# Kernel optimization log

Hardware: AMD Instinct MI355X
Metric: run time of the kernel (lower is better)

## Reference

```python
import jax, jax.numpy as jnp
import numpy as np

VOCAB, H, L, B, T = 32000, 256, 10, 256, 512


def setup_inputs() -> dict:
    key = jax.random.key(0)
    ks = jax.random.split(key, 6)
    s = 1.0 / np.sqrt(H)
    return {
        "tokens": jax.random.randint(ks[0], (B, T), 0, VOCAB),
        "hidden0": jnp.zeros((L, B, H), jnp.float32),
        "emb": jax.random.normal(ks[1], (VOCAB, H), jnp.float32),
        "Wx_w": jax.random.normal(ks[2], (L, H, H), jnp.float32) * s,
        "Wx_b": jax.random.normal(ks[3], (L, H), jnp.float32) * s,
        "Wh_w": jax.random.normal(ks[4], (L, H, H), jnp.float32) * s,
        "Wh_b": jax.random.normal(ks[5], (L, H), jnp.float32) * s,
    }


def reference(tokens, hidden0, emb, Wx_w, Wx_b, Wh_w, Wh_b):
    # tokens: [B,T] int; hidden0: [L,B,H]; weights stacked over layers.
    embedded = emb[tokens]                    # [B,T,H]
    xs = jnp.swapaxes(embedded, 0, 1)         # [T,B,H]

    def time_step(h, x_t):                    # h: [L,B,H], x_t: [B,H]
        def layer_step(x, layer):
            wx, bx, wh, bh, hl = layer
            # torch Linear: y = x @ W.T + b
            new_h = jnp.tanh(x @ wx.T + bx + hl @ wh.T + bh)
            return new_h, new_h
        x_out, new_h = jax.lax.scan(layer_step, x_t, (Wx_w, Wx_b, Wh_w, Wh_b, h))
        return new_h, x_out                   # carry new hidden stack, emit top-layer output

    h_final, outs = jax.lax.scan(time_step, hidden0, xs)  # outs: [T,B,H]
    return jnp.swapaxes(outs, 0, 1), h_final  # ([B,T,H], [L,B,H])
```

## Files before the change

### kernel.cpp

```cpp
#include <hip/hip_runtime.h>

#define HDIM   256
#define NLAYER 10
#define BATCH  256
#define TSTEPS 512
#define NTHR   512
#define DEPTH  8
#define NCH    160
#define NWG    160

typedef __attribute__((ext_vector_type(8))) short short8;
typedef __attribute__((ext_vector_type(4))) float f32x4;

__device__ __forceinline__ unsigned short bf16_rne(float f) {
    unsigned v = __float_as_uint(f);
    unsigned r = v + 0x7FFFu + ((v >> 16) & 1u);
    return (unsigned short)(r >> 16);
}
__device__ __forceinline__ float bf16_f(unsigned short b) {
    return __uint_as_float(((unsigned)b) << 16);
}
__device__ __forceinline__ float fast_tanh(float v) {
    float a = fabsf(v);
    float e = __expf(-2.0f * a);
    float r = (1.0f - e) / (1.0f + e);
    return __builtin_copysignf(r, v);
}
__device__ __forceinline__ void cvt8(const float* __restrict__ p, short8& hi, short8& lo) {
#pragma unroll
    for (int e = 0; e < 8; ++e) {
        float f = p[e];
        unsigned short h = bf16_rne(f);
        hi[e] = (short)h;
        lo[e] = (short)bf16_rne(f - bf16_f(h));
    }
}
__device__ __forceinline__ void cvtq(unsigned long long q0, unsigned long long q1,
                                     unsigned long long q2, unsigned long long q3,
                                     short8& hi, short8& lo) {
    unsigned long long q[4] = { q0, q1, q2, q3 };
#pragma unroll
    for (int i = 0; i < 4; ++i) {
#pragma unroll
        for (int j = 0; j < 2; ++j) {
            const float f = __uint_as_float((unsigned)(q[i] >> (32 * j)));
            const unsigned short h = bf16_rne(f);
            hi[2 * i + j] = (short)h;
            lo[2 * i + j] = (short)bf16_rne(f - bf16_f(h));
        }
    }
}
__device__ __forceinline__ void unpack8(unsigned long long q0, unsigned long long q1,
                                        unsigned long long q2, unsigned long long q3,
                                        short8& hi, short8& lo) {
    unsigned long long q[4] = { q0, q1, q2, q3 };
#pragma unroll
    for (int i = 0; i < 4; ++i) {
        unsigned u0 = (unsigned)q[i], u1 = (unsigned)(q[i] >> 32);
        hi[2 * i]     = (short)(u0 & 0xffffu); lo[2 * i]     = (short)(u0 >> 16);
        hi[2 * i + 1] = (short)(u1 & 0xffffu); lo[2 * i + 1] = (short)(u1 >> 16);
    }
}

#define MFMA16(a, b, c) __builtin_amdgcn_mfma_f32_16x16x32_bf16((a), (b), (c), 0, 0, 0)

__device__ __forceinline__ void wait_ge(int* f, int need) {
    while (__hip_atomic_load(f, __ATOMIC_RELAXED, __HIP_MEMORY_SCOPE_AGENT) < need)
        __builtin_amdgcn_s_sleep(1);
}
#define AT_LD(p)    __hip_atomic_load((p), __ATOMIC_RELAXED, __HIP_MEMORY_SCOPE_AGENT)
#define AT_ST(p, v) __hip_atomic_store((p), (v), __ATOMIC_RELAXED, __HIP_MEMORY_SCOPE_AGENT)
#define VMDRAIN()   asm volatile("s_waitcnt vmcnt(0)" ::: "memory")

#define WXH 0
#define HHI 131072
#define HLO 139264
#define XHI 147456
#define XLO 155648

__global__ void __launch_bounds__(NTHR, 1) rnn_fused(
    const int* __restrict__ tokens, const float* __restrict__ hidden0,
    const float* __restrict__ emb,
    const float* __restrict__ Wx_w, const float* __restrict__ Wx_b,
    const float* __restrict__ Wh_w, const float* __restrict__ Wh_b,
    unsigned* __restrict__ hg,
    int* __restrict__ fh,
    float* __restrict__ out) {
    const int bid = blockIdx.x;
    const int l = bid >> 4;
    const int s16 = bid & 15;
    const int c = bid;
    const int tid = threadIdx.x;
    const int wv = tid >> 6;
    const int lane = tid & 63;
    const int ln15 = lane & 15;
    const int kq = (lane >> 4) << 3;
    const int hi16 = (lane >> 4) << 4;
    const int swz = (ln15 & 7) << 4;
    const int srow = tid >> 5;
    const int scb = tid & 31;

    __shared__ char smem[163840];
    float* hfinal = out + (size_t)BATCH * TSTEPS * HDIM;

    {
        const float* wxsrcA = Wx_w + (size_t)l * 65536;
        for (int i = 0; i < 16; ++i) {
            const int ch = tid + i * NTHR;
            const int r = ch >> 5, kb = ch & 31;
            short8 hi, lo;
            cvt8(wxsrcA + (size_t)r * HDIM + kb * 8, hi, lo);
            *(short8*)(smem + WXH + r * 512 + ((kb * 16) ^ ((r & 7) << 4))) = hi;
        }
    }
    short8 whh[2][8], whl[2][8], wxl[2][8];
    {
        const float* whsrc = Wh_w + (size_t)l * 65536;
        const float* wxsrc = Wx_w + (size_t)l * 65536;
#define WINIT(ni, kc) do { \
        short8 _d; \
        cvt8(whsrc + (size_t)(wv * 32 + ni * 16 + ln15) * HDIM + kc * 32 + kq, whh[ni][kc], whl[ni][kc]); \
        cvt8(wxsrc + (size_t)(wv * 32 + ni * 16 + ln15) * HDIM + kc * 32 + kq, _d, wxl[ni][kc]); \
        asm volatile("" : "+v"(whh[ni][kc]), "+v"(whl[ni][kc]), "+v"(wxl[ni][kc])); \
    } while (0)
        WINIT(0,0); WINIT(0,1); WINIT(0,2); WINIT(0,3);
        WINIT(0,4); WINIT(0,5); WINIT(0,6); WINIT(0,7);
        WINIT(1,0); WINIT(1,1); WINIT(1,2); WINIT(1,3);
        WINIT(1,4); WINIT(1,5); WINIT(1,6); WINIT(1,7);
#undef WINIT
    }
    {
        short8 hi, lo;
        cvt8(hidden0 + ((size_t)(l * BATCH + s16 * 16 + srow)) * HDIM + scb * 8, hi, lo);
        const int so = srow * 512 + ((scb * 16) ^ ((srow & 7) << 4));
        *(short8*)(smem + HHI + so) = hi;
        *(short8*)(smem + HLO + so) = lo;
    }
    float bv[2];
#pragma unroll
    for (int ni = 0; ni < 2; ++ni) {
        const int col = wv * 32 + ni * 16 + ln15;
        bv[ni] = Wx_b[l * HDIM + col] + Wh_b[l * HDIM + col];
    }

    int* fhme = fh + (size_t)c * TSTEPS;
    int* fhp = (l > 0) ? fh + (size_t)(c - 16) * TSTEPS : nullptr;
    int* fhn = (l < NLAYER - 1) ? fh + (size_t)(c + 16) * TSTEPS : nullptr;

    if (l > 0) {
        if (tid == 0) wait_ge(fhp + 0, 1);
        __syncthreads();
        unsigned long long* xp = (unsigned long long*)
            (hg + ((size_t)0 * NCH + (c - 16)) * 4096) + (size_t)tid * 4;
        unsigned long long q0 = AT_LD(xp), q1 = AT_LD(xp + 1),
                           q2 = AT_LD(xp + 2), q3 = AT_LD(xp + 3);
        short8 sxh, sxl;
        unpack8(q0, q1, q2, q3, sxh, sxl);
        const int so = srow * 512 + ((scb * 16) ^ ((srow & 7) << 4));
        *(short8*)(smem + XHI + so) = sxh;
        *(short8*)(smem + XLO + so) = sxl;
    } else {
        const int tok = tokens[(s16 * 16 + srow) * TSTEPS + 0];
        const float* ep = emb + (size_t)tok * HDIM + scb * 8;
        short8 sxh, sxl;
        cvt8(ep, sxh, sxl);
        const int so = srow * 512 + ((scb * 16) ^ ((srow & 7) << 4));
        *(short8*)(smem + XHI + so) = sxh;
        *(short8*)(smem + XLO + so) = sxl;
    }
    __syncthreads();

    for (int t = 0; t < TSTEPS; ++t) {
        if (tid == 0 && l > 0 && t + 1 < TSTEPS) wait_ge(fhp + (t + 1), 1);
        if (tid == 64 && fhn && t >= 9) wait_ge(fhn + (t - 9), 1);
        __syncthreads();

        unsigned long long q0 = 0, q1 = 0, q2 = 0, q3 = 0;
        if (t + 1 < TSTEPS) {
            if (l > 0) {
                unsigned long long* xp = (unsigned long long*)
                    (hg + ((size_t)((t + 1) % DEPTH) * NCH + (c - 16)) * 4096) + (size_t)tid * 4;
                q0 = AT_LD(xp); q1 = AT_LD(xp + 1); q2 = AT_LD(xp + 2); q3 = AT_LD(xp + 3);
            } else {
                const int tok = tokens[(s16 * 16 + srow) * TSTEPS + (t + 1)];
                const unsigned long long* ep =
                    (const unsigned long long*)(emb + (size_t)tok * HDIM + scb * 8);
                q0 = ep[0]; q1 = ep[1]; q2 = ep[2]; q3 = ep[3];
            }
        }

        f32x4 acc0 = {}, acc1 = {};
#define HX_KC(kc) do { \
        const int _off = ((kc) * 64 + hi16) ^ swz; \
        const short8 hh  = *(const short8*)(smem + HHI + ln15 * 512 + _off); \
        const short8 hl  = *(const short8*)(smem + HLO + ln15 * 512 + _off); \
        const short8 xh  = *(const short8*)(smem + XHI + ln15 * 512 + _off); \
        const short8 xl  = *(const short8*)(smem + XLO + ln15 * 512 + _off); \
        const short8 bh0 = *(const short8*)(smem + WXH + (wv * 32 + ln15) * 512 + _off); \
        const short8 bh1 = *(const short8*)(smem + WXH + (wv * 32 + 16 + ln15) * 512 + _off); \
        acc0 = MFMA16(hh, whh[0][kc], acc0);  acc1 = MFMA16(hh, whh[1][kc], acc1); \
        acc0 = MFMA16(hh, whl[0][kc], acc0);  acc1 = MFMA16(hh, whl[1][kc], acc1); \
        acc0 = MFMA16(hl, whh[0][kc], acc0);  acc1 = MFMA16(hl, whh[1][kc], acc1); \
        acc0 = MFMA16(xh, bh0, acc0);         acc1 = MFMA16(xh, bh1, acc1); \
        acc0 = MFMA16(xh, wxl[0][kc], acc0);  acc1 = MFMA16(xh, wxl[1][kc], acc1); \
        acc0 = MFMA16(xl, bh0, acc0);         acc1 = MFMA16(xl, bh1, acc1); \
    } while (0)
        HX_KC(0); HX_KC(1); HX_KC(2); HX_KC(3);
        HX_KC(4); HX_KC(5); HX_KC(6); HX_KC(7);
#undef HX_KC

        unsigned pk[2][4];
#pragma unroll
        for (int ni = 0; ni < 2; ++ni) {
            const f32x4 a = (ni == 0) ? acc0 : acc1;
#pragma unroll
            for (int r = 0; r < 4; ++r) {
                const float y = fast_tanh(a[r] + bv[ni]);
                const unsigned short yh = bf16_rne(y);
                const unsigned short yl = bf16_rne(y - bf16_f(yh));
                pk[ni][r] = (unsigned)yh | ((unsigned)yl << 16);
            }
        }

        VMDRAIN();
        __syncthreads();

        if (tid == 0 && t > 0)
            AT_ST(fhme + (t - 1), 1);
        {
            unsigned* hgw = (fhn) ? hg + ((size_t)(t % DEPTH) * NCH + c) * 4096 : nullptr;
#pragma unroll
            for (int ni = 0; ni < 2; ++ni) {
                const int col = wv * 32 + ni * 16 + ln15;
#pragma unroll
                for (int r = 0; r < 4; ++r) {
                    const int row = ((lane >> 4) << 2) + r;
                    const int so = row * 512 + ((2 * col) ^ ((row & 7) << 4));
                    *(unsigned short*)(smem + HHI + so) = (unsigned short)(pk[ni][r] & 0xffffu);
                    *(unsigned short*)(smem + HLO + so) = (unsigned short)(pk[ni][r] >> 16);
                    if (hgw) {
                        AT_ST(hgw + (size_t)row * HDIM + col, pk[ni][r]);
                    } else {
                        const float y = bf16_f((unsigned short)(pk[ni][r] & 0xffffu)) +
                                        bf16_f((unsigned short)(pk[ni][r] >> 16));
                        out[((size_t)(s16 * 16 + row) * TSTEPS + t) * HDIM + col] = y;
                    }
                    if (t == TSTEPS - 1) {
                        const float y = bf16_f((unsigned short)(pk[ni][r] & 0xffffu)) +
                                        bf16_f((unsigned short)(pk[ni][r] >> 16));
                        hfinal[((size_t)l * BATCH + s16 * 16 + row) * HDIM + col] = y;
                    }
                }
            }
            if (t + 1 < TSTEPS) {
                short8 sxh, sxl;
                if (l > 0) unpack8(q0, q1, q2, q3, sxh, sxl);
                else       cvtq(q0, q1, q2, q3, sxh, sxl);
                const int so = srow * 512 + ((scb * 16) ^ ((srow & 7) << 4));
                *(short8*)(smem + XHI + so) = sxh;
                *(short8*)(smem + XLO + so) = sxl;
            }
        }
    }
    VMDRAIN();
    __syncthreads();
    if (tid == 0) AT_ST(fhme + (TSTEPS - 1), 1);
}

extern "C" void kernel_launch(void* const* d_in, const int* in_sizes, int n_in,
                              void* d_out, int out_size, void* d_ws, size_t ws_size,
                              hipStream_t stream) {
    const int* tokens = (const int*)d_in[0];
    const float* hidden0 = (const float*)d_in[1];
    const float* emb = (const float*)d_in[2];
    const float* Wx_w = (const float*)d_in[3];
    const float* Wx_b = (const float*)d_in[4];
    const float* Wh_w = (const float*)d_in[5];
    const float* Wh_b = (const float*)d_in[6];
    float* out = (float*)d_out;

    char* ws = (char*)d_ws;
    size_t off = 0;
    auto carve = [&](size_t bytes) -> void* {
        void* p = ws + off;
        off = (off + bytes + 255) & ~(size_t)255;
        return p;
    };
    unsigned* hg = (unsigned*)carve((size_t)DEPTH * NCH * 16 * HDIM * 4);
    int* fh = (int*)carve((size_t)NCH * TSTEPS * 4);
    (void)ws_size; (void)in_sizes; (void)n_in; (void)out_size;

    hipMemsetAsync(fh, 0, (size_t)NCH * TSTEPS * 4, stream);

    void* args[] = { (void*)&tokens, (void*)&hidden0, (void*)&emb,
                     (void*)&Wx_w, (void*)&Wx_b, (void*)&Wh_w, (void*)&Wh_b,
                     (void*)&hg, (void*)&fh, (void*)&out };
    hipLaunchCooperativeKernel((void*)rnn_fused, dim3(NWG), dim3(NTHR), args, 0, stream);
}
```

Before: 3.426 ms.

## Have each layer precompute next layer's input projection and add embedding-feed workgroups

```diff
diff --git a/kernel.cpp b/kernel.cpp
--- a/kernel.cpp
+++ b/kernel.cpp
@@ -6,8 +6,9 @@
 #define TSTEPS 512
 #define NTHR   512
 #define DEPTH  8
-#define NCH    160
-#define NWG    160
+#define NREC   160
+#define NFEED  16
+#define NWG    176
 
 typedef __attribute__((ext_vector_type(8))) short short8;
 typedef __attribute__((ext_vector_type(4))) float f32x4;
@@ -35,32 +36,6 @@
         lo[e] = (short)bf16_rne(f - bf16_f(h));
     }
 }
-__device__ __forceinline__ void cvtq(unsigned long long q0, unsigned long long q1,
-                                     unsigned long long q2, unsigned long long q3,
-                                     short8& hi, short8& lo) {
-    unsigned long long q[4] = { q0, q1, q2, q3 };
-#pragma unroll
-    for (int i = 0; i < 4; ++i) {
-#pragma unroll
-        for (int j = 0; j < 2; ++j) {
-            const float f = __uint_as_float((unsigned)(q[i] >> (32 * j)));
-            const unsigned short h = bf16_rne(f);
-            hi[2 * i + j] = (short)h;
-            lo[2 * i + j] = (short)bf16_rne(f - bf16_f(h));
-        }
-    }
-}
-__device__ __forceinline__ void unpack8(unsigned long long q0, unsigned long long q1,
-                                        unsigned long long q2, unsigned long long q3,
-                                        short8& hi, short8& lo) {
-    unsigned long long q[4] = { q0, q1, q2, q3 };
-#pragma unroll
-    for (int i = 0; i < 4; ++i) {
-        unsigned u0 = (unsigned)q[i], u1 = (unsigned)(q[i] >> 32);
-        hi[2 * i]     = (short)(u0 & 0xffffu); lo[2 * i]     = (short)(u0 >> 16);
-        hi[2 * i + 1] = (short)(u1 & 0xffffu); lo[2 * i + 1] = (short)(u1 >> 16);
-    }
-}
 
 #define MFMA16(a, b, c) __builtin_amdgcn_mfma_f32_16x16x32_bf16((a), (b), (c), 0, 0, 0)
 
@@ -71,25 +46,32 @@
 #define AT_LD(p)    __hip_atomic_load((p), __ATOMIC_RELAXED, __HIP_MEMORY_SCOPE_AGENT)
 #define AT_ST(p, v) __hip_atomic_store((p), (v), __ATOMIC_RELAXED, __HIP_MEMORY_SCOPE_AGENT)
 #define VMDRAIN()   asm volatile("s_waitcnt vmcnt(0)" ::: "memory")
+#define PKF(a, b)   (((unsigned long long)__float_as_uint(b) << 32) | __float_as_uint(a))
 
 #define WXH 0
 #define HHI 131072
 #define HLO 139264
-#define XHI 147456
-#define XLO 155648
-
-__global__ void __launch_bounds__(NTHR, 1) rnn_fused(
+
+__device__ __forceinline__ void stage_whi_f32(const float* __restrict__ src, char* smem, int tid) {
+    for (int i = 0; i < 16; ++i) {
+        const int ch = tid + i * NTHR;
+        const int r = ch >> 5, kb = ch & 31;
+        short8 hi, lo;
+        cvt8(src + (size_t)r * HDIM + kb * 8, hi, lo);
+        *(short8*)(smem + r * 512 + ((kb * 16) ^ ((r & 7) << 4))) = hi;
+    }
+}
+
+__global__ void __launch_bounds__(NTHR) rnn_pipe(
     const int* __restrict__ tokens, const float* __restrict__ hidden0,
     const float* __restrict__ emb,
     const float* __restrict__ Wx_w, const float* __restrict__ Wx_b,
     const float* __restrict__ Wh_w, const float* __restrict__ Wh_b,
-    unsigned* __restrict__ hg,
-    int* __restrict__ fh,
+    float* __restrict__ u,
+    int* __restrict__ fu,
+    int* __restrict__ fd,
     float* __restrict__ out) {
     const int bid = blockIdx.x;
-    const int l = bid >> 4;
-    const int s16 = bid & 15;
-    const int c = bid;
     const int tid = threadIdx.x;
     const int wv = tid >> 6;
     const int lane = tid & 63;
@@ -100,135 +82,117 @@
     const int srow = tid >> 5;
     const int scb = tid & 31;
 
-    __shared__ char smem[163840];
+    __shared__ char smem[147456];
     float* hfinal = out + (size_t)BATCH * TSTEPS * HDIM;
 
-    {
-        const float* wxsrcA = Wx_w + (size_t)l * 65536;
-        for (int i = 0; i < 16; ++i) {
-            const int ch = tid + i * NTHR;
-            const int r = ch >> 5, kb = ch & 31;
+    if (bid < NREC) {
+        const int l = bid >> 4, s16 = bid & 15;
+        const bool ship = (l < NLAYER - 1);
+
+        if (ship) stage_whi_f32(Wx_w + (size_t)(l + 1) * 65536, smem, tid);
+        short8 whh[2][8], whl[2][8], wxl[2][8];
+        {
+            const float* whsrc = Wh_w + (size_t)l * 65536;
+            const float* wxsrc = Wx_w + (size_t)(l + 1) * 65536;
+#define WINIT(ni, kc) do { \
+            cvt8(whsrc + (size_t)(wv * 32 + ni * 16 + ln15) * HDIM + kc * 32 + kq, whh[ni][kc], whl[ni][kc]); \
+            if (ship) { short8 _d; \
+                cvt8(wxsrc + (size_t)(wv * 32 + ni * 16 + ln15) * HDIM + kc * 32 + kq, _d, wxl[ni][kc]); } \
+            else { wxl[ni][kc] = short8{0,0,0,0,0,0,0,0}; } \
+            asm volatile("" : "+v"(whh[ni][kc]), "+v"(whl[ni][kc]), "+v"(wxl[ni][kc])); \
+        } while (0)
+            WINIT(0,0); WINIT(0,1); WINIT(0,2); WINIT(0,3);
+            WINIT(0,4); WINIT(0,5); WINIT(0,6); WINIT(0,7);
+            WINIT(1,0); WINIT(1,1); WINIT(1,2); WINIT(1,3);
+            WINIT(1,4); WINIT(1,5); WINIT(1,6); WINIT(1,7);
+#undef WINIT
+        }
+        {
             short8 hi, lo;
-            cvt8(wxsrcA + (size_t)r * HDIM + kb * 8, hi, lo);
-            *(short8*)(smem + WXH + r * 512 + ((kb * 16) ^ ((r & 7) << 4))) = hi;
-        }
-    }
-    short8 whh[2][8], whl[2][8], wxl[2][8];
-    {
-        const float* whsrc = Wh_w + (size_t)l * 65536;
-        const float* wxsrc = Wx_w + (size_t)l * 65536;
-#define WINIT(ni, kc) do { \
-        short8 _d; \
-        cvt8(whsrc + (size_t)(wv * 32 + ni * 16 + ln15) * HDIM + kc * 32 + kq, whh[ni][kc], whl[ni][kc]); \
-        cvt8(wxsrc + (size_t)(wv * 32 + ni * 16 + ln15) * HDIM + kc * 32 + kq, _d, wxl[ni][kc]); \
-        asm volatile("" : "+v"(whh[ni][kc]), "+v"(whl[ni][kc]), "+v"(wxl[ni][kc])); \
-    } while (0)
-        WINIT(0,0); WINIT(0,1); WINIT(0,2); WINIT(0,3);
-        WINIT(0,4); WINIT(0,5); WINIT(0,6); WINIT(0,7);
-        WINIT(1,0); WINIT(1,1); WINIT(1,2); WINIT(1,3);
-        WINIT(1,4); WINIT(1,5); WINIT(1,6); WINIT(1,7);
-#undef WINIT
-    }
-    {
-        short8 hi, lo;
-        cvt8(hidden0 + ((size_t)(l * BATCH + s16 * 16 + srow)) * HDIM + scb * 8, hi, lo);
-        const int so = srow * 512 + ((scb * 16) ^ ((srow & 7) << 4));
-        *(short8*)(smem + HHI + so) = hi;
-        *(short8*)(smem + HLO + so) = lo;
-    }
-    float bv[2];
-#pragma unroll
-    for (int ni = 0; ni < 2; ++ni) {
-        const int col = wv * 32 + ni * 16 + ln15;
-        bv[ni] = Wx_b[l * HDIM + col] + Wh_b[l * HDIM + col];
-    }
-
-    int* fhme = fh + (size_t)c * TSTEPS;
-    int* fhp = (l > 0) ? fh + (size_t)(c - 16) * TSTEPS : nullptr;
-    int* fhn = (l < NLAYER - 1) ? fh + (size_t)(c + 16) * TSTEPS : nullptr;
-
-    if (l > 0) {
-        if (tid == 0) wait_ge(fhp + 0, 1);
+            cvt8(hidden0 + ((size_t)(l * BATCH + s16 * 16 + srow)) * HDIM + scb * 8, hi, lo);
+            const int so = srow * 512 + ((scb * 16) ^ ((srow & 7) << 4));
+            *(short8*)(smem + HHI + so) = hi;
+            *(short8*)(smem + HLO + so) = lo;
+        }
+        float bvn[2] = { 0.f, 0.f };
+        if (ship) {
+#pragma unroll
+            for (int ni = 0; ni < 2; ++ni) {
+                const int col = wv * 32 + ni * 16 + ln15;
+                bvn[ni] = Wx_b[(l + 1) * HDIM + col] + Wh_b[(l + 1) * HDIM + col];
+            }
+        }
+
+        int* fuMe = fu + ((size_t)l * 16 + s16) * TSTEPS;
+        int* fuNx = ship ? fu + ((size_t)(l + 1) * 16 + s16) * TSTEPS : nullptr;
+        int* fuG  = (l < NLAYER - 2) ? fu + ((size_t)(l + 2) * 16 + s16) * TSTEPS : nullptr;
+        int* fdA  = fd + (size_t)s16 * TSTEPS;
+        const unsigned long long* myu = (const unsigned long long*)
+            (u + ((size_t)l * 16 + s16) * DEPTH * 4096);
+        unsigned long long* nxu = ship ? (unsigned long long*)
+            (u + ((size_t)(l + 1) * 16 + s16) * DEPTH * 4096) : nullptr;
+
         __syncthreads();
-        unsigned long long* xp = (unsigned long long*)
-            (hg + ((size_t)0 * NCH + (c - 16)) * 4096) + (size_t)tid * 4;
-        unsigned long long q0 = AT_LD(xp), q1 = AT_LD(xp + 1),
-                           q2 = AT_LD(xp + 2), q3 = AT_LD(xp + 3);
-        short8 sxh, sxl;
-        unpack8(q0, q1, q2, q3, sxh, sxl);
-        const int so = srow * 512 + ((scb * 16) ^ ((srow & 7) << 4));
-        *(short8*)(smem + XHI + so) = sxh;
-        *(short8*)(smem + XLO + so) = sxl;
-    } else {
-        const int tok = tokens[(s16 * 16 + srow) * TSTEPS + 0];
-        const float* ep = emb + (size_t)tok * HDIM + scb * 8;
-        short8 sxh, sxl;
-        cvt8(ep, sxh, sxl);
-        const int so = srow * 512 + ((scb * 16) ^ ((srow & 7) << 4));
-        *(short8*)(smem + XHI + so) = sxh;
-        *(short8*)(smem + XLO + so) = sxl;
-    }
-    __syncthreads();
-
-    for (int t = 0; t < TSTEPS; ++t) {
-        if (tid == 0 && l > 0 && t + 1 < TSTEPS) wait_ge(fhp + (t + 1), 1);
-        if (tid == 64 && fhn && t >= 9) wait_ge(fhn + (t - 9), 1);
-        __syncthreads();
-
-        unsigned long long q0 = 0, q1 = 0, q2 = 0, q3 = 0;
-        if (t + 1 < TSTEPS) {
-            if (l > 0) {
-                unsigned long long* xp = (unsigned long long*)
-                    (hg + ((size_t)((t + 1) % DEPTH) * NCH + (c - 16)) * 4096) + (size_t)tid * 4;
-                q0 = AT_LD(xp); q1 = AT_LD(xp + 1); q2 = AT_LD(xp + 2); q3 = AT_LD(xp + 3);
-            } else {
-                const int tok = tokens[(s16 * 16 + srow) * TSTEPS + (t + 1)];
-                const unsigned long long* ep =
-                    (const unsigned long long*)(emb + (size_t)tok * HDIM + scb * 8);
-                q0 = ep[0]; q1 = ep[1]; q2 = ep[2]; q3 = ep[3];
-            }
-        }
-
-        f32x4 acc0 = {}, acc1 = {};
-#define HX_KC(kc) do { \
-        const int _off = ((kc) * 64 + hi16) ^ swz; \
-        const short8 hh  = *(const short8*)(smem + HHI + ln15 * 512 + _off); \
-        const short8 hl  = *(const short8*)(smem + HLO + ln15 * 512 + _off); \
-        const short8 xh  = *(const short8*)(smem + XHI + ln15 * 512 + _off); \
-        const short8 xl  = *(const short8*)(smem + XLO + ln15 * 512 + _off); \
-        const short8 bh0 = *(const short8*)(smem + WXH + (wv * 32 + ln15) * 512 + _off); \
-        const short8 bh1 = *(const short8*)(smem + WXH + (wv * 32 + 16 + ln15) * 512 + _off); \
-        acc0 = MFMA16(hh, whh[0][kc], acc0);  acc1 = MFMA16(hh, whh[1][kc], acc1); \
-        acc0 = MFMA16(hh, whl[0][kc], acc0);  acc1 = MFMA16(hh, whl[1][kc], acc1); \
-        acc0 = MFMA16(hl, whh[0][kc], acc0);  acc1 = MFMA16(hl, whh[1][kc], acc1); \
-        acc0 = MFMA16(xh, bh0, acc0);         acc1 = MFMA16(xh, bh1, acc1); \
-        acc0 = MFMA16(xh, wxl[0][kc], acc0);  acc1 = MFMA16(xh, wxl[1][kc], acc1); \
-        acc0 = MFMA16(xl, bh0, acc0);         acc1 = MFMA16(xl, bh1, acc1); \
-    } while (0)
-        HX_KC(0); HX_KC(1); HX_KC(2); HX_KC(3);
-        HX_KC(4); HX_KC(5); HX_KC(6); HX_KC(7);
+
+        for (int t = 0; t < TSTEPS; ++t) {
+            if (tid == 0) wait_ge(fuMe + t, 1);
+            if (tid == 64 && ship) {
+                if (l < NLAYER - 2) { if (t >= 11) wait_ge(fuG + (t - 11), 1); }
+                else                { if (t >= 9)  wait_ge(fdA + (t - 9), 1); }
+            }
+            __syncthreads();
+
+            const unsigned long long* up = myu + (size_t)(t & 7) * 2048 + (size_t)tid * 4;
+            unsigned long long q0 = AT_LD(up), q1 = AT_LD(up + 1),
+                               q2 = AT_LD(up + 2), q3 = AT_LD(up + 3);
+
+            const bool doU = ship && (t >= 1);
+            f32x4 ah0a = {}, ah0b = {}, ah1a = {}, ah1b = {};
+            f32x4 au0 = {}, au1 = {};
+#define HX_KC(kc, A0, A1) do { \
+            const int _off = ((kc) * 64 + hi16) ^ swz; \
+            const short8 hh = *(const short8*)(smem + HHI + ln15 * 512 + _off); \
+            const short8 hl = *(const short8*)(smem + HLO + ln15 * 512 + _off); \
+            A0 = MFMA16(hh, whh[0][kc], A0);  A1 = MFMA16(hh, whh[1][kc], A1); \
+            A0 = MFMA16(hh, whl[0][kc], A0);  A1 = MFMA16(hh, whl[1][kc], A1); \
+            A0 = MFMA16(hl, whh[0][kc], A0);  A1 = MFMA16(hl, whh[1][kc], A1); \
+            if (doU) { \
+                const short8 bh0 = *(const short8*)(smem + WXH + (wv * 32 + ln15) * 512 + _off); \
+                const short8 bh1 = *(const short8*)(smem + WXH + (wv * 32 + 16 + ln15) * 512 + _off); \
+                au0 = MFMA16(hh, bh0, au0);         au1 = MFMA16(hh, bh1, au1); \
+                au0 = MFMA16(hh, wxl[0][kc], au0);  au1 = MFMA16(hh, wxl[1][kc], au1); \
+                au0 = MFMA16(hl, bh0, au0);         au1 = MFMA16(hl, bh1, au1); \
+            } \
+        } while (0)
+            HX_KC(0, ah0a, ah1a); HX_KC(1, ah0a, ah1a);
+            HX_KC(2, ah0a, ah1a); HX_KC(3, ah0a, ah1a);
+            HX_KC(4, ah0b, ah1b); HX_KC(5, ah0b, ah1b);
+            HX_KC(6, ah0b, ah1b); HX_KC(7, ah0b, ah1b);
 #undef HX_KC
 
-        unsigned pk[2][4];
-#pragma unroll
-        for (int ni = 0; ni < 2; ++ni) {
-            const f32x4 a = (ni == 0) ? acc0 : acc1;
-#pragma unroll
-            for (int r = 0; r < 4; ++r) {
-                const float y = fast_tanh(a[r] + bv[ni]);
-                const unsigned short yh = bf16_rne(y);
-                const unsigned short yl = bf16_rne(y - bf16_f(yh));
-                pk[ni][r] = (unsigned)yh | ((unsigned)yl << 16);
-            }
-        }
-
-        VMDRAIN();
-        __syncthreads();
-
-        if (tid == 0 && t > 0)
-            AT_ST(fhme + (t - 1), 1);
-        {
-            unsigned* hgw = (fhn) ? hg + ((size_t)(t % DEPTH) * NCH + c) * 4096 : nullptr;
+            VMDRAIN();
+            __syncthreads();
+
+            if (tid == 0) {
+                if (ship && t >= 2) AT_ST(fuNx + (t - 2), 1);
+                if (!ship) AT_ST(fdA + t, 1);
+            }
+            unsigned pk[2][4];
+            {
+                const float uv[2][4] = {
+                    { __uint_as_float((unsigned)q0), __uint_as_float((unsigned)(q0 >> 32)),
+                      __uint_as_float((unsigned)q1), __uint_as_float((unsigned)(q1 >> 32)) },
+                    { __uint_as_float((unsigned)q2), __uint_as_float((unsigned)(q2 >> 32)),
+                      __uint_as_float((unsigned)q3), __uint_as_float((unsigned)(q3 >> 32)) } };
+#pragma unroll
+                for (int r = 0; r < 4; ++r) {
+                    const float y0 = fast_tanh(ah0a[r] + ah0b[r] + uv[0][r]);
+                    const float y1 = fast_tanh(ah1a[r] + ah1b[r] + uv[1][r]);
+                    unsigned short h0 = bf16_rne(y0), h1 = bf16_rne(y1);
+                    pk[0][r] = (unsigned)h0 | ((unsigned)bf16_rne(y0 - bf16_f(h0)) << 16);
+                    pk[1][r] = (unsigned)h1 | ((unsigned)bf16_rne(y1 - bf16_f(h1)) << 16);
+                }
+            }
 #pragma unroll
             for (int ni = 0; ni < 2; ++ni) {
                 const int col = wv * 32 + ni * 16 + ln15;
@@ -238,9 +202,7 @@
                     const int so = row * 512 + ((2 * col) ^ ((row & 7) << 4));
                     *(unsigned short*)(smem + HHI + so) = (unsigned short)(pk[ni][r] & 0xffffu);
                     *(unsigned short*)(smem + HLO + so) = (unsigned short)(pk[ni][r] >> 16);
-                    if (hgw) {
-                        AT_ST(hgw + (size_t)row * HDIM + col, pk[ni][r]);
-                    } else {
+                    if (!ship) {
                         const float y = bf16_f((unsigned short)(pk[ni][r] & 0xffffu)) +
                                         bf16_f((unsigned short)(pk[ni][r] >> 16));
                         out[((size_t)(s16 * 16 + row) * TSTEPS + t) * HDIM + col] = y;
@@ -252,19 +214,109 @@
                     }
                 }
             }
-            if (t + 1 < TSTEPS) {
-                short8 sxh, sxl;
-                if (l > 0) unpack8(q0, q1, q2, q3, sxh, sxl);
-                else       cvtq(q0, q1, q2, q3, sxh, sxl);
+            if (doU) {
+                unsigned long long* us = nxu + (size_t)((t - 1) & 7) * 2048 + (size_t)tid * 4;
+                AT_ST(us + 0, PKF(au0[0] + bvn[0], au0[1] + bvn[0]));
+                AT_ST(us + 1, PKF(au0[2] + bvn[0], au0[3] + bvn[0]));
+                AT_ST(us + 2, PKF(au1[0] + bvn[1], au1[1] + bvn[1]));
+                AT_ST(us + 3, PKF(au1[2] + bvn[1], au1[3] + bvn[1]));
+            }
+        }
+
+        if (ship) {
+            if (tid == 64) {
+                if (l < NLAYER - 2) wait_ge(fuG + 501, 1);
+                else                wait_ge(fdA + 503, 1);
+            }
+            __syncthreads();
+            f32x4 au0 = {}, au1 = {};
+#define UE_KC(kc) do { \
+            const int _off = ((kc) * 64 + hi16) ^ swz; \
+            const short8 hh = *(const short8*)(smem + HHI + ln15 * 512 + _off); \
+            const short8 hl = *(const short8*)(smem + HLO + ln15 * 512 + _off); \
+            const short8 bh0 = *(const short8*)(smem + WXH + (wv * 32 + ln15) * 512 + _off); \
+            const short8 bh1 = *(const short8*)(smem + WXH + (wv * 32 + 16 + ln15) * 512 + _off); \
+            au0 = MFMA16(hh, bh0, au0);         au1 = MFMA16(hh, bh1, au1); \
+            au0 = MFMA16(hh, wxl[0][kc], au0);  au1 = MFMA16(hh, wxl[1][kc], au1); \
+            au0 = MFMA16(hl, bh0, au0);         au1 = MFMA16(hl, bh1, au1); \
+        } while (0)
+            UE_KC(0); UE_KC(1); UE_KC(2); UE_KC(3);
+            UE_KC(4); UE_KC(5); UE_KC(6); UE_KC(7);
+#undef UE_KC
+            unsigned long long* us = nxu + (size_t)(511 & 7) * 2048 + (size_t)tid * 4;
+            AT_ST(us + 0, PKF(au0[0] + bvn[0], au0[1] + bvn[0]));
+            AT_ST(us + 1, PKF(au0[2] + bvn[0], au0[3] + bvn[0]));
+            AT_ST(us + 2, PKF(au1[0] + bvn[1], au1[1] + bvn[1]));
+            AT_ST(us + 3, PKF(au1[2] + bvn[1], au1[3] + bvn[1]));
+            VMDRAIN();
+            __syncthreads();
+            if (tid == 0) {
+                AT_ST(fuNx + 510, 1);
+                AT_ST(fuNx + 511, 1);
+            }
+        }
+    } else {
+        const int s16 = bid - NREC;
+        stage_whi_f32(Wx_w, smem, tid);
+        short8 wxl[2][8];
+#define FWINIT(ni, kc) do { \
+        short8 _d; \
+        cvt8(Wx_w + (size_t)(wv * 32 + ni * 16 + ln15) * HDIM + kc * 32 + kq, _d, wxl[ni][kc]); \
+        asm volatile("" : "+v"(wxl[ni][kc])); \
+    } while (0)
+        FWINIT(0,0); FWINIT(0,1); FWINIT(0,2); FWINIT(0,3);
+        FWINIT(0,4); FWINIT(0,5); FWINIT(0,6); FWINIT(0,7);
+        FWINIT(1,0); FWINIT(1,1); FWINIT(1,2); FWINIT(1,3);
+        FWINIT(1,4); FWINIT(1,5); FWINIT(1,6); FWINIT(1,7);
+#undef FWINIT
+        float b0[2];
+#pragma unroll
+        for (int ni = 0; ni < 2; ++ni) {
+            const int col = wv * 32 + ni * 16 + ln15;
+            b0[ni] = Wx_b[col] + Wh_b[col];
+        }
+        int* fuMe = fu + (size_t)s16 * TSTEPS;
+        int* fuG  = fu + ((size_t)16 + s16) * TSTEPS;
+        unsigned long long* nxu = (unsigned long long*)
+            (u + (size_t)s16 * DEPTH * 4096);
+        __syncthreads();
+
+        for (int t = 0; t < TSTEPS; ++t) {
+            if (tid == 0 && t >= 10) wait_ge(fuG + (t - 10), 1);
+            __syncthreads();
+            {
+                const int tok = tokens[(s16 * 16 + srow) * TSTEPS + t];
+                short8 hi, lo;
+                cvt8(emb + (size_t)tok * HDIM + scb * 8, hi, lo);
                 const int so = srow * 512 + ((scb * 16) ^ ((srow & 7) << 4));
-                *(short8*)(smem + XHI + so) = sxh;
-                *(short8*)(smem + XLO + so) = sxl;
-            }
+                *(short8*)(smem + HHI + so) = hi;
+                *(short8*)(smem + HLO + so) = lo;
+            }
+            __syncthreads();
+            f32x4 ax0 = {}, ax1 = {};
+#define FX_KC(kc) do { \
+            const int _off = ((kc) * 64 + hi16) ^ swz; \
+            const short8 xh = *(const short8*)(smem + HHI + ln15 * 512 + _off); \
+            const short8 xl = *(const short8*)(smem + HLO + ln15 * 512 + _off); \
+            const short8 bh0 = *(const short8*)(smem + WXH + (wv * 32 + ln15) * 512 + _off); \
+            const short8 bh1 = *(const short8*)(smem + WXH + (wv * 32 + 16 + ln15) * 512 + _off); \
+            ax0 = MFMA16(xh, bh0, ax0);         ax1 = MFMA16(xh, bh1, ax1); \
+            ax0 = MFMA16(xh, wxl[0][kc], ax0);  ax1 = MFMA16(xh, wxl[1][kc], ax1); \
+            ax0 = MFMA16(xl, bh0, ax0);         ax1 = MFMA16(xl, bh1, ax1); \
+        } while (0)
+            FX_KC(0); FX_KC(1); FX_KC(2); FX_KC(3);
+            FX_KC(4); FX_KC(5); FX_KC(6); FX_KC(7);
+#undef FX_KC
+            unsigned long long* us = nxu + (size_t)(t & 7) * 2048 + (size_t)tid * 4;
+            AT_ST(us + 0, PKF(ax0[0] + b0[0], ax0[1] + b0[0]));
+            AT_ST(us + 1, PKF(ax0[2] + b0[0], ax0[3] + b0[0]));
+            AT_ST(us + 2, PKF(ax1[0] + b0[1], ax1[1] + b0[1]));
+            AT_ST(us + 3, PKF(ax1[2] + b0[1], ax1[3] + b0[1]));
+            VMDRAIN();
+            __syncthreads();
+            if (tid == 0) AT_ST(fuMe + t, 1);
         }
     }
-    VMDRAIN();
-    __syncthreads();
-    if (tid == 0) AT_ST(fhme + (TSTEPS - 1), 1);
 }
 
 extern "C" void kernel_launch(void* const* d_in, const int* in_sizes, int n_in,
@@ -286,14 +338,15 @@
         off = (off + bytes + 255) & ~(size_t)255;
         return p;
     };
-    unsigned* hg = (unsigned*)carve((size_t)DEPTH * NCH * 16 * HDIM * 4);
-    int* fh = (int*)carve((size_t)NCH * TSTEPS * 4);
+    float* u = (float*)carve((size_t)NLAYER * 16 * DEPTH * 4096 * 4);
+    int* fu = (int*)carve((size_t)NLAYER * 16 * TSTEPS * 4);
+    int* fd = (int*)carve((size_t)16 * TSTEPS * 4);
     (void)ws_size; (void)in_sizes; (void)n_in; (void)out_size;
 
-    hipMemsetAsync(fh, 0, (size_t)NCH * TSTEPS * 4, stream);
+    hipMemsetAsync(fu, 0, (size_t)(NLAYER * 16 + 16) * TSTEPS * 4, stream);
 
     void* args[] = { (void*)&tokens, (void*)&hidden0, (void*)&emb,
                      (void*)&Wx_w, (void*)&Wx_b, (void*)&Wh_w, (void*)&Wh_b,
-                     (void*)&hg, (void*)&fh, (void*)&out };
-    hipLaunchCooperativeKernel((void*)rnn_fused, dim3(NWG), dim3(NTHR), args, 0, stream);
-}
+                     (void*)&u, (void*)&fu, (void*)&fd, (void*)&out };
+    hipLaunchCooperativeKernel((void*)rnn_pipe, dim3(NWG), dim3(NTHR), args, 0, stream);
+}
```

New measurement: 3.372 ms. Within noise of the previous version (-1.6%).
